# Performance work log

Measured on AMD Instinct MI355X. Metric: run time of the kernel, lower is better.

## Reference

```python
import jax, jax.numpy as jnp
import numpy as np

ENC_DIM, DEC_DIM, ATT_DIM = 2048, 512, 512
B, N = 256, 196


def setup_inputs() -> dict:
    key = jax.random.key(0)
    ks = jax.random.split(key, 8)
    s_enc = 1.0 / np.sqrt(ENC_DIM)
    s_dec = 1.0 / np.sqrt(DEC_DIM)
    s_full = 1.0 / np.sqrt(ATT_DIM)
    return {
        "encoder_out": jax.random.normal(ks[0], (B, N, ENC_DIM), jnp.float32),
        "hidden": jax.random.normal(ks[1], (B, DEC_DIM), jnp.float32),
        "W_enc": jax.random.uniform(ks[2], (ENC_DIM, ATT_DIM), jnp.float32, -s_enc, s_enc),
        "b_enc": jax.random.uniform(ks[3], (ATT_DIM,), jnp.float32, -s_enc, s_enc),
        "W_dec": jax.random.uniform(ks[4], (DEC_DIM, ATT_DIM), jnp.float32, -s_dec, s_dec),
        "b_dec": jax.random.uniform(ks[5], (ATT_DIM,), jnp.float32, -s_dec, s_dec),
        "W_full": jax.random.uniform(ks[6], (ATT_DIM, 1), jnp.float32, -s_full, s_full),
        "b_full": jax.random.uniform(ks[7], (1,), jnp.float32, -s_full, s_full),
    }


def reference(encoder_out, hidden, W_enc, b_enc, W_dec, b_dec, W_full, b_full):
    # enc proj: [B, N, A]; dec proj: [B, 1, A] broadcast over pixels
    att1 = jnp.einsum('bne,ea->bna', encoder_out, W_enc) + b_enc
    att2 = hidden @ W_dec + b_dec                       # [B, A]
    att = jax.nn.relu(att1 + att2[:, None, :])          # [B, N, A]
    scores = (jnp.einsum('bna,a->bn', att, W_full[:, 0]) + b_full[0])  # [B, N]
    alpha = jax.nn.softmax(scores, axis=1)              # softmax over pixels
    context = jnp.einsum('bne,bn->be', encoder_out, alpha)  # [B, E]
    return (context, alpha)
```

## Files before the change

### kernel.cpp

```cpp
#include <hip/hip_runtime.h>
#include <hip/hip_bf16.h>
#include <stdint.h>

#define ENC_DIM 2048
#define ATT_DIM 512
#define BATCH   256
#define NPIX    196
#define MTOT    (BATCH*NPIX)
#define CTX_OFF (BATCH*ENC_DIM)
#define KC      32
#define NCHUNK  (ENC_DIM/KC)

typedef __attribute__((ext_vector_type(8))) short  short8;
typedef __attribute__((ext_vector_type(4))) float  f32x4;

__device__ __forceinline__ unsigned int f2bf(float x) {
    union { float f; uint32_t u; } v; v.f = x;
    return (v.u + 0x7FFFu + ((v.u >> 16) & 1u)) >> 16;
}

__device__ __forceinline__ void gll16(const void* g, void* l) {
    __builtin_amdgcn_global_load_lds(
        (const __attribute__((address_space(1))) unsigned int*)g,
        (__attribute__((address_space(3))) unsigned int*)l, 16, 0, 0);
}

__global__ __launch_bounds__(256) void pack_wenc(const float* __restrict__ W,
                                                 unsigned short* __restrict__ Wp) {
    const int i  = blockIdx.x * 256 + threadIdx.x;
    const int n  = i & 511;
    const int kg = i >> 9;
    short8 v;
#pragma unroll
    for (int j = 0; j < 8; ++j)
        v[j] = (short)f2bf(W[(size_t)(kg * 8 + j) * 512 + n]);
    *(short8*)(Wp + (size_t)i * 8) = v;
}

__global__ __launch_bounds__(256) void att2_kernel(const float* __restrict__ hidden,
                                                   const float* __restrict__ Wdec,
                                                   const float* __restrict__ bdec,
                                                   const float* __restrict__ benc,
                                                   float* __restrict__ att2p) {
    __shared__ float h[512];
    const int b   = blockIdx.x;
    const int tid = threadIdx.x;
    h[tid]       = hidden[(size_t)b * 512 + tid];
    h[tid + 256] = hidden[(size_t)b * 512 + tid + 256];
    __syncthreads();
    float acc0 = bdec[tid]       + benc[tid];
    float acc1 = bdec[tid + 256] + benc[tid + 256];
#pragma unroll 4
    for (int k = 0; k < 512; ++k) {
        const float hk = h[k];
        acc0 = fmaf(hk, Wdec[(size_t)k * 512 + tid],       acc0);
        acc1 = fmaf(hk, Wdec[(size_t)k * 512 + tid + 256], acc1);
    }
    att2p[(size_t)b * 512 + tid]       = acc0;
    att2p[(size_t)b * 512 + tid + 256] = acc1;
}

__global__ __launch_bounds__(512, 4) void score_kernel(const float* __restrict__ enc,
                                                       const unsigned short* __restrict__ Wp,
                                                       const float* __restrict__ att2p,
                                                       const float* __restrict__ Wfull,
                                                       float* __restrict__ scores) {
    __shared__ __align__(16) unsigned short ldsA[2][64 * KC];
    __shared__ __align__(16) unsigned short ldsB[2][4 * 512 * 8];
    __shared__ float lds_att2[2][ATT_DIM];
    __shared__ float lds_wf[ATT_DIM];
    __shared__ float lds_sc[64];

    const int tid = threadIdx.x;
    const int w   = tid >> 6;
    const int l   = tid & 63;
    const int m0  = blockIdx.x * 64;
    const int b0  = m0 / NPIX;
    const int b1  = (m0 + 63) / NPIX;

    lds_att2[0][tid] = att2p[(size_t)b0 * ATT_DIM + tid];
    lds_att2[1][tid] = att2p[(size_t)b1 * ATT_DIM + tid];
    lds_wf[tid] = Wfull[tid];
    if (tid < 64) lds_sc[tid] = 0.0f;

    f32x4 acc[4][4];
#pragma unroll
    for (int i = 0; i < 4; ++i)
#pragma unroll
        for (int j = 0; j < 4; ++j)
            acc[i][j] = (f32x4){0.f, 0.f, 0.f, 0.f};

    const int ar  = tid >> 3;
    const int ah  = tid & 7;
    const int axr = (ar >> 1) & 3;
    const float* aG = enc + (size_t)(m0 + ar) * ENC_DIM + ah * 4;
    const int a_wr_off = ar * KC + ((ah >> 1) ^ axr) * 8 + (ah & 1) * 4;

    const unsigned char* WpB = (const unsigned char*)Wp;

    int a_rd[4], b_rd[4];
#pragma unroll
    for (int mf = 0; mf < 4; ++mf) {
        const int r = mf * 16 + (l & 15);
        a_rd[mf] = r * KC + (((l >> 4) ^ ((r >> 1) & 3)) * 8);
    }
#pragma unroll
    for (int nf = 0; nf < 4; ++nf) {
        const int col = w * 64 + nf * 16 + (l & 15);
        b_rd[nf] = ((l >> 4) * 512 + col) * 8;
    }

#pragma unroll
    for (int it = 0; it < 4; ++it) {
        const int seg = w * 4 + it;
        gll16(WpB + (size_t)seg * 1024 + l * 16,
              (unsigned char*)ldsB[0] + seg * 1024 + l * 16);
    }
    {
        f32x4 a0 = *(const f32x4*)aG;
        uint32_t* dst = (uint32_t*)(ldsA[0] + a_wr_off);
        dst[0] = f2bf(a0[0]) | (f2bf(a0[1]) << 16);
        dst[1] = f2bf(a0[2]) | (f2bf(a0[3]) << 16);
    }
    __syncthreads();

#pragma unroll 2
    for (int c = 0; c < NCHUNK - 1; ++c) {
        const int p = c & 1;
#pragma unroll
        for (int it = 0; it < 4; ++it) {
            const int seg = w * 4 + it;
            gll16(WpB + (size_t)(c + 1) * 32768 + seg * 1024 + l * 16,
                  (unsigned char*)ldsB[p ^ 1] + seg * 1024 + l * 16);
        }
        f32x4 an = *(const f32x4*)(aG + (c + 1) * KC);
        short8 af[4], bfv[4];
#pragma unroll
        for (int mf = 0; mf < 4; ++mf) af[mf]  = *(const short8*)(ldsA[p] + a_rd[mf]);
#pragma unroll
        for (int nf = 0; nf < 4; ++nf) bfv[nf] = *(const short8*)(ldsB[p] + b_rd[nf]);
#pragma unroll
        for (int mf = 0; mf < 4; ++mf)
#pragma unroll
            for (int nf = 0; nf < 4; ++nf)
                acc[mf][nf] = __builtin_amdgcn_mfma_f32_16x16x32_bf16(
                    af[mf], bfv[nf], acc[mf][nf], 0, 0, 0);
        {
            uint32_t* dst = (uint32_t*)(ldsA[p ^ 1] + a_wr_off);
            dst[0] = f2bf(an[0]) | (f2bf(an[1]) << 16);
            dst[1] = f2bf(an[2]) | (f2bf(an[3]) << 16);
        }
        __syncthreads();
    }
    {
        const int p = (NCHUNK - 1) & 1;
        short8 af[4], bfv[4];
#pragma unroll
        for (int mf = 0; mf < 4; ++mf) af[mf]  = *(const short8*)(ldsA[p] + a_rd[mf]);
#pragma unroll
        for (int nf = 0; nf < 4; ++nf) bfv[nf] = *(const short8*)(ldsB[p] + b_rd[nf]);
#pragma unroll
        for (int mf = 0; mf < 4; ++mf)
#pragma unroll
            for (int nf = 0; nf < 4; ++nf)
                acc[mf][nf] = __builtin_amdgcn_mfma_f32_16x16x32_bf16(
                    af[mf], bfv[nf], acc[mf][nf], 0, 0, 0);
    }

#pragma unroll
    for (int mf = 0; mf < 4; ++mf) {
#pragma unroll
        for (int reg = 0; reg < 4; ++reg) {
            const int row = mf * 16 + ((l >> 4) << 2) + reg;
            const int sel = ((m0 + row) >= (b0 + 1) * NPIX) ? 1 : 0;
            float sv = 0.0f;
#pragma unroll
            for (int nf = 0; nf < 4; ++nf) {
                const int col = (w << 6) + (nf << 4) + (l & 15);
                float v = acc[mf][nf][reg] + lds_att2[sel][col];
                v = fmaxf(v, 0.0f);
                sv = fmaf(v, lds_wf[col], sv);
            }
            sv += __shfl_xor(sv, 8);
            sv += __shfl_xor(sv, 4);
            sv += __shfl_xor(sv, 2);
            sv += __shfl_xor(sv, 1);
            if ((l & 15) == 0) atomicAdd(&lds_sc[row], sv);
        }
    }
    __syncthreads();
    if (tid < 64) scores[m0 + tid] = lds_sc[tid];
}

__global__ __launch_bounds__(256) void ctx_kernel(const float* __restrict__ enc,
                                                  const float* __restrict__ scores,
                                                  float* __restrict__ out) {
    __shared__ float salpha[NPIX];
    __shared__ float red[8];
    __shared__ float partial[512];
    const int tid  = threadIdx.x;
    const int lane = tid & 63;
    const int wid  = tid >> 6;
    const int b    = blockIdx.x >> 2;
    const int eq   = blockIdx.x & 3;

    const float sv = (tid < NPIX) ? scores[(size_t)b * NPIX + tid] : -1e30f;
    float mx = sv;
#pragma unroll
    for (int m = 32; m >= 1; m >>= 1) mx = fmaxf(mx, __shfl_xor(mx, m));
    if (lane == 0) red[wid] = mx;
    __syncthreads();
    if (tid == 0) red[4] = fmaxf(fmaxf(red[0], red[1]), fmaxf(red[2], red[3]));
    __syncthreads();
    const float bm = red[4];
    const float ex = (tid < NPIX) ? __expf(sv - bm) : 0.0f;
    float sm = ex;
#pragma unroll
    for (int m = 32; m >= 1; m >>= 1) sm += __shfl_xor(sm, m);
    if (lane == 0) red[wid] = sm;
    __syncthreads();
    if (tid == 0) red[5] = red[0] + red[1] + red[2] + red[3];
    __syncthreads();
    const float inv = 1.0f / red[5];
    if (tid < NPIX) {
        const float av = ex * inv;
        salpha[tid] = av;
        if (eq == 0) out[CTX_OFF + (size_t)b * NPIX + tid] = av;
    }
    __syncthreads();

    const int l128 = tid & 127;
    const int ph   = tid >> 7;
    const float* ep = enc + (size_t)b * NPIX * ENC_DIM + eq * 512 + l128 * 4;
    f32x4 acc = (f32x4){0.f, 0.f, 0.f, 0.f};
#pragma unroll 4
    for (int n = ph; n < NPIX; n += 2) {
        const float al = salpha[n];
        f32x4 v = *(const f32x4*)(ep + (size_t)n * ENC_DIM);
        acc += v * al;
    }
    if (ph == 1) *(f32x4*)(partial + l128 * 4) = acc;
    __syncthreads();
    if (ph == 0) {
        f32x4 o = acc + *(const f32x4*)(partial + l128 * 4);
        *(f32x4*)(out + (size_t)b * ENC_DIM + eq * 512 + l128 * 4) = o;
    }
}

extern "C" void kernel_launch(void* const* d_in, const int* in_sizes, int n_in,
                              void* d_out, int out_size, void* d_ws, size_t ws_size,
                              hipStream_t stream) {
    const float* enc    = (const float*)d_in[0];
    const float* hidden = (const float*)d_in[1];
    const float* Wenc   = (const float*)d_in[2];
    const float* benc   = (const float*)d_in[3];
    const float* Wdec   = (const float*)d_in[4];
    const float* bdec   = (const float*)d_in[5];
    const float* Wfull  = (const float*)d_in[6];
    float* out = (float*)d_out;

    unsigned short* Wp    = (unsigned short*)d_ws;
    float*          att2p = (float*)((char*)d_ws + (2u << 20));
    float*          scores= (float*)((char*)d_ws + (2u << 20) + (512u << 10));

    pack_wenc  <<<512, 256, 0, stream>>>(Wenc, Wp);
    att2_kernel<<<BATCH, 256, 0, stream>>>(hidden, Wdec, bdec, benc, att2p);
    score_kernel<<<MTOT / 64, 512, 0, stream>>>(enc, Wp, att2p, Wfull, scores);
    ctx_kernel <<<BATCH * 4, 256, 0, stream>>>(enc, scores, out);
}
```

Measured before the change: 335.6 us.

## Load packed W_enc fragments directly to registers and double K chunk to 64

The score GEMM no longer stages W_enc tiles in LDS with global_load_lds. Each wave now reads its bf16 B fragments straight from global memory (expected to hit L2) into registers. The K chunk grows from 32 to 64, which halves the number of barriers, and the A tile uses a new XOR swizzle with 16-byte stores. Occupancy hint drops from 4 to 3 blocks, the loop is no longer unrolled, and B loads are not prefetched ahead, so global latency may be exposed right before the MFMAs.

```diff
diff --git a/kernel.cpp b/kernel.cpp
--- a/kernel.cpp
+++ b/kernel.cpp
@@ -6,23 +6,17 @@
 #define ATT_DIM 512
 #define BATCH   256
 #define NPIX    196
-#define MTOT    (BATCH*NPIX)
+#define MROWS   (BATCH*NPIX)
 #define CTX_OFF (BATCH*ENC_DIM)
-#define KC      32
-#define NCHUNK  (ENC_DIM/KC)
+#define KC      64
+#define NCH     (ENC_DIM/KC)
 
 typedef __attribute__((ext_vector_type(8))) short  short8;
 typedef __attribute__((ext_vector_type(4))) float  f32x4;
 
-__device__ __forceinline__ unsigned int f2bf(float x) {
+__device__ __forceinline__ uint32_t f2bf(float x) {
     union { float f; uint32_t u; } v; v.f = x;
     return (v.u + 0x7FFFu + ((v.u >> 16) & 1u)) >> 16;
-}
-
-__device__ __forceinline__ void gll16(const void* g, void* l) {
-    __builtin_amdgcn_global_load_lds(
-        (const __attribute__((address_space(1))) unsigned int*)g,
-        (__attribute__((address_space(3))) unsigned int*)l, 16, 0, 0);
 }
 
 __global__ __launch_bounds__(256) void pack_wenc(const float* __restrict__ W,
@@ -60,13 +54,12 @@
     att2p[(size_t)b * 512 + tid + 256] = acc1;
 }
 
-__global__ __launch_bounds__(512, 4) void score_kernel(const float* __restrict__ enc,
+__global__ __launch_bounds__(512, 3) void score_kernel(const float* __restrict__ enc,
                                                        const unsigned short* __restrict__ Wp,
                                                        const float* __restrict__ att2p,
                                                        const float* __restrict__ Wfull,
                                                        float* __restrict__ scores) {
-    __shared__ __align__(16) unsigned short ldsA[2][64 * KC];
-    __shared__ __align__(16) unsigned short ldsB[2][4 * 512 * 8];
+    __shared__ __align__(16) unsigned char ldsA[2][64 * KC * 2];
     __shared__ float lds_att2[2][ATT_DIM];
     __shared__ float lds_wf[ATT_DIM];
     __shared__ float lds_sc[64];
@@ -83,6 +76,25 @@
     lds_wf[tid] = Wfull[tid];
     if (tid < 64) lds_sc[tid] = 0.0f;
 
+    const int arow = tid >> 3;
+    const int akg  = tid & 7;
+    const int awr  = arow * 128 + ((akg ^ (arow & 7)) << 4);
+    const float* aG = enc + (size_t)(m0 + arow) * ENC_DIM + akg * 8;
+
+    int ard[4], akey[4];
+#pragma unroll
+    for (int mf = 0; mf < 4; ++mf) {
+        const int r = mf * 16 + (l & 15);
+        ard[mf]  = r * 128;
+        akey[mf] = r & 7;
+    }
+    const int kq = l >> 4;
+
+    int boff[4];
+#pragma unroll
+    for (int nf = 0; nf < 4; ++nf)
+        boff[nf] = (kq * 512 + (w << 6) + (nf << 4) + (l & 15)) * 8;
+
     f32x4 acc[4][4];
 #pragma unroll
     for (int i = 0; i < 4; ++i)
@@ -90,82 +102,59 @@
         for (int j = 0; j < 4; ++j)
             acc[i][j] = (f32x4){0.f, 0.f, 0.f, 0.f};
 
-    const int ar  = tid >> 3;
-    const int ah  = tid & 7;
-    const int axr = (ar >> 1) & 3;
-    const float* aG = enc + (size_t)(m0 + ar) * ENC_DIM + ah * 4;
-    const int a_wr_off = ar * KC + ((ah >> 1) ^ axr) * 8 + (ah & 1) * 4;
-
-    const unsigned char* WpB = (const unsigned char*)Wp;
-
-    int a_rd[4], b_rd[4];
-#pragma unroll
-    for (int mf = 0; mf < 4; ++mf) {
-        const int r = mf * 16 + (l & 15);
-        a_rd[mf] = r * KC + (((l >> 4) ^ ((r >> 1) & 3)) * 8);
-    }
-#pragma unroll
-    for (int nf = 0; nf < 4; ++nf) {
-        const int col = w * 64 + nf * 16 + (l & 15);
-        b_rd[nf] = ((l >> 4) * 512 + col) * 8;
-    }
-
-#pragma unroll
-    for (int it = 0; it < 4; ++it) {
-        const int seg = w * 4 + it;
-        gll16(WpB + (size_t)seg * 1024 + l * 16,
-              (unsigned char*)ldsB[0] + seg * 1024 + l * 16);
-    }
     {
         f32x4 a0 = *(const f32x4*)aG;
-        uint32_t* dst = (uint32_t*)(ldsA[0] + a_wr_off);
-        dst[0] = f2bf(a0[0]) | (f2bf(a0[1]) << 16);
-        dst[1] = f2bf(a0[2]) | (f2bf(a0[3]) << 16);
-    }
-    __syncthreads();
-
-#pragma unroll 2
-    for (int c = 0; c < NCHUNK - 1; ++c) {
+        f32x4 a1 = *(const f32x4*)(aG + 4);
+        uint4 u;
+        u.x = f2bf(a0[0]) | (f2bf(a0[1]) << 16);
+        u.y = f2bf(a0[2]) | (f2bf(a0[3]) << 16);
+        u.z = f2bf(a1[0]) | (f2bf(a1[1]) << 16);
+        u.w = f2bf(a1[2]) | (f2bf(a1[3]) << 16);
+        *(uint4*)(ldsA[0] + awr) = u;
+    }
+    __syncthreads();
+
+#define STEP(S, BV)                                                            \
+    {                                                                          \
+        _Pragma("unroll")                                                      \
+        for (int mf = 0; mf < 4; ++mf) {                                       \
+            short8 af = *(const short8*)(ldsR + ard[mf] +                      \
+                                         ((((S) * 4 + kq) ^ akey[mf]) << 4));  \
+            _Pragma("unroll")                                                  \
+            for (int nf = 0; nf < 4; ++nf)                                     \
+                acc[mf][nf] = __builtin_amdgcn_mfma_f32_16x16x32_bf16(         \
+                    af, BV[nf], acc[mf][nf], 0, 0, 0);                         \
+        }                                                                      \
+    }
+
+#pragma unroll 1
+    for (int c = 0; c < NCH; ++c) {
         const int p = c & 1;
-#pragma unroll
-        for (int it = 0; it < 4; ++it) {
-            const int seg = w * 4 + it;
-            gll16(WpB + (size_t)(c + 1) * 32768 + seg * 1024 + l * 16,
-                  (unsigned char*)ldsB[p ^ 1] + seg * 1024 + l * 16);
+        const unsigned char* ldsR = ldsA[p];
+        const unsigned short* bC  = Wp + (size_t)c * 32768;
+        short8 b0v[4], b1v[4];
+#pragma unroll
+        for (int nf = 0; nf < 4; ++nf) b0v[nf] = *(const short8*)(bC + boff[nf]);
+#pragma unroll
+        for (int nf = 0; nf < 4; ++nf) b1v[nf] = *(const short8*)(bC + boff[nf] + 16384);
+        f32x4 an0, an1;
+        if (c < NCH - 1) {
+            an0 = *(const f32x4*)(aG + (c + 1) * KC);
+            an1 = *(const f32x4*)(aG + (c + 1) * KC + 4);
         }
-        f32x4 an = *(const f32x4*)(aG + (c + 1) * KC);
-        short8 af[4], bfv[4];
-#pragma unroll
-        for (int mf = 0; mf < 4; ++mf) af[mf]  = *(const short8*)(ldsA[p] + a_rd[mf]);
-#pragma unroll
-        for (int nf = 0; nf < 4; ++nf) bfv[nf] = *(const short8*)(ldsB[p] + b_rd[nf]);
-#pragma unroll
-        for (int mf = 0; mf < 4; ++mf)
-#pragma unroll
-            for (int nf = 0; nf < 4; ++nf)
-                acc[mf][nf] = __builtin_amdgcn_mfma_f32_16x16x32_bf16(
-                    af[mf], bfv[nf], acc[mf][nf], 0, 0, 0);
-        {
-            uint32_t* dst = (uint32_t*)(ldsA[p ^ 1] + a_wr_off);
-            dst[0] = f2bf(an[0]) | (f2bf(an[1]) << 16);
-            dst[1] = f2bf(an[2]) | (f2bf(an[3]) << 16);
+        STEP(0, b0v)
+        if (c < NCH - 1) {
+            uint4 u;
+            u.x = f2bf(an0[0]) | (f2bf(an0[1]) << 16);
+            u.y = f2bf(an0[2]) | (f2bf(an0[3]) << 16);
+            u.z = f2bf(an1[0]) | (f2bf(an1[1]) << 16);
+            u.w = f2bf(an1[2]) | (f2bf(an1[3]) << 16);
+            *(uint4*)(ldsA[p ^ 1] + awr) = u;
         }
+        STEP(1, b1v)
         __syncthreads();
     }
-    {
-        const int p = (NCHUNK - 1) & 1;
-        short8 af[4], bfv[4];
-#pragma unroll
-        for (int mf = 0; mf < 4; ++mf) af[mf]  = *(const short8*)(ldsA[p] + a_rd[mf]);
-#pragma unroll
-        for (int nf = 0; nf < 4; ++nf) bfv[nf] = *(const short8*)(ldsB[p] + b_rd[nf]);
-#pragma unroll
-        for (int mf = 0; mf < 4; ++mf)
-#pragma unroll
-            for (int nf = 0; nf < 4; ++nf)
-                acc[mf][nf] = __builtin_amdgcn_mfma_f32_16x16x32_bf16(
-                    af[mf], bfv[nf], acc[mf][nf], 0, 0, 0);
-    }
+#undef STEP
 
 #pragma unroll
     for (int mf = 0; mf < 4; ++mf) {
@@ -263,8 +252,8 @@
     float*          att2p = (float*)((char*)d_ws + (2u << 20));
     float*          scores= (float*)((char*)d_ws + (2u << 20) + (512u << 10));
 
-    pack_wenc  <<<512, 256, 0, stream>>>(Wenc, Wp);
-    att2_kernel<<<BATCH, 256, 0, stream>>>(hidden, Wdec, bdec, benc, att2p);
-    score_kernel<<<MTOT / 64, 512, 0, stream>>>(enc, Wp, att2p, Wfull, scores);
-    ctx_kernel <<<BATCH * 4, 256, 0, stream>>>(enc, scores, out);
-}
+    pack_wenc   <<<512, 256, 0, stream>>>(Wenc, Wp);
+    att2_kernel <<<BATCH, 256, 0, stream>>>(hidden, Wdec, bdec, benc, att2p);
+    score_kernel<<<MROWS / 64, 512, 0, stream>>>(enc, Wp, att2p, Wfull, scores);
+    ctx_kernel  <<<BATCH * 4, 256, 0, stream>>>(enc, scores, out);
+}
```

After: 313.4 us. 6.6% less time.
